# Optimization experiments

Hardware: AMD Instinct MI355X
Metric: run time of the kernel (lower is better)

Reference implementation:

```python
import jax, jax.numpy as jnp
import numpy as np

B, S, H, A = 32, 2048, 1024, 256
NEG = jnp.float32(-1e20)


def setup_inputs() -> dict:
    key = jax.random.key(0)
    k = jax.random.split(key, 6)
    h_i = jax.random.normal(k[0], (B, S, H), jnp.float32)
    h_t = jax.random.normal(k[1], (B, H), jnp.float32)
    mask = jax.random.randint(k[2], (B, S), 0, 2).astype(bool)
    W = jax.random.normal(k[3], (A, 2 * H), jnp.float32) * 0.02
    b = jax.random.normal(k[4], (A,), jnp.float32) * 0.02
    u = jax.random.normal(k[5], (A, 1), jnp.float32)
    return {"h_i": h_i, "h_t": h_t, "mask": mask, "W": W, "b": b, "u": u}


def reference(h_i, h_t, mask, W, b, u):
    Bn, Sn, Hn = h_i.shape
    # h_t expanded along seq and concatenated: [B,S,2H]
    h_t_e = jnp.broadcast_to(h_t[:, None, :], (Bn, Sn, Hn))
    comb = jnp.concatenate([h_i, h_t_e], axis=-1)
    m = jnp.tanh(jnp.einsum('bsk,ak->bsa', comb, W) + b)  # [B,S,A]
    y = jnp.einsum('bsa,a->bs', m, u[:, 0])                # raw scores [B,S]
    # Faithful replication of torch masked_scatter per time step over the batch
    # dim: at step s, the masked batch positions receive SUCCESSIVE elements of
    # the score column y[:, s] (not necessarily the positionally aligned ones).
    pos = jnp.clip(jnp.cumsum(mask.astype(jnp.int32), axis=0) - 1, 0)  # [B,S]
    y_scattered = jnp.take_along_axis(y, pos, axis=0)
    beta = jnp.where(mask, y_scattered, NEG)
    alpha = jax.nn.softmax(beta, axis=1)                   # softmax over seq
    s = jnp.einsum('bs,bsh->bh', alpha, h_i)               # weighted sum [B,H]
    return s
```

## Files before the change

### kernel.cpp

```cpp
#include <hip/hip_runtime.h>
#include <math.h>

#define BB 32
#define SS 2048
#define HH 1024
#define AA 256
#define NEGV (-1e20f)
#define BK 32
#define NT (HH / BK)
#define NG 16

typedef _Float16 half8 __attribute__((ext_vector_type(8)));
typedef float f32x4 __attribute__((ext_vector_type(4)));

__device__ inline void async_lds16(const void* g, void* l) {
    __builtin_amdgcn_global_load_lds(
        (const __attribute__((address_space(1))) unsigned int*)g,
        (__attribute__((address_space(3))) unsigned int*)l, 16, 0, 0);
}

__device__ inline f32x4 gload4(const float* p) {
    f32x4 r;
    asm volatile("global_load_dwordx4 %0, %1, off"
                 : "=&v"(r) : "v"(p) : "memory");
    return r;
}

__device__ inline half8 cvt8(f32x4 a, f32x4 b) {
    half8 h;
    h[0] = (_Float16)a[0]; h[1] = (_Float16)a[1];
    h[2] = (_Float16)a[2]; h[3] = (_Float16)a[3];
    h[4] = (_Float16)b[0]; h[5] = (_Float16)b[1];
    h[6] = (_Float16)b[2]; h[7] = (_Float16)b[3];
    return h;
}
__device__ inline half8 cvt8f(float4 a, float4 b) {
    half8 h;
    h[0] = (_Float16)a.x; h[1] = (_Float16)a.y;
    h[2] = (_Float16)a.z; h[3] = (_Float16)a.w;
    h[4] = (_Float16)b.x; h[5] = (_Float16)b.y;
    h[6] = (_Float16)b.z; h[7] = (_Float16)b.w;
    return h;
}

__global__ __launch_bounds__(256) void k_prep(const float* __restrict__ W,
                                              const float* __restrict__ h_t,
                                              const float* __restrict__ bias,
                                              const int* __restrict__ mask,
                                              _Float16* __restrict__ W16t,
                                              float* __restrict__ c,
                                              int* __restrict__ sList,
                                              int* __restrict__ cntb,
                                              int* __restrict__ pcnt,
                                              float* __restrict__ out) {
    const int blk = blockIdx.x;
    const int tid = threadIdx.x;
    __shared__ int lcnt;

    if (blk < 128) {
        int idx = blk * 256 + tid;
        int kt = idx >> 10;
        int u  = idx & 1023;
        int col = u >> 2, ks = u & 3;
        const float* src = W + (size_t)col * 2 * HH + kt * BK + ks * 8;
        float4 a0 = *(const float4*)src;
        float4 a1 = *(const float4*)(src + 4);
        *reinterpret_cast<half8*>(W16t + (size_t)idx * 8) = cvt8f(a0, a1);
        return;
    }
    if (blk < 2176) {
        int wave = tid >> 6;
        int lane = tid & 63;
        int pair = (blk - 128) * 4 + wave;
        int b = pair >> 8;
        int a = pair & (AA - 1);
        const float* ht = h_t + (size_t)b * HH;
        const float* w2 = W + (size_t)a * 2 * HH + HH;
        float acc = 0.f;
        for (int k = lane; k < HH; k += 64)
            acc += ht[k] * w2[k];
        for (int off = 32; off; off >>= 1)
            acc += __shfl_down(acc, off, 64);
        if (lane == 0) c[pair] = acc + bias[a];
        return;
    }
    if (blk >= 2208) {
        int i = (blk - 2208) * 256 + tid;
        *reinterpret_cast<f32x4*>(&out[(size_t)i * 4]) = (f32x4){0.f, 0.f, 0.f, 0.f};
        return;
    }
    const int b = blk - 2176;
    const int lane = tid & 63;
    if (tid == 0) lcnt = 0;
    __syncthreads();
    int* lst = sList + b * SS;
#pragma unroll
    for (int i = 0; i < 8; ++i) {
        int s = tid + i * 256;
        int pref = 0, tot = 0;
#pragma unroll
        for (int bb = 0; bb < BB; ++bb) {
            int mv = (mask[bb * SS + s] != 0);
            tot += mv;
            if (bb <= b) pref += mv;
        }
        pcnt[b * SS + s] = pref;
        bool need = (tot > b);
        unsigned long long mk = __ballot(need);
        int wbase = 0;
        if (lane == 0) wbase = atomicAdd(&lcnt, __popcll(mk));
        wbase = __shfl(wbase, 0, 64);
        if (need) lst[wbase + __popcll(mk & ((1ull << lane) - 1))] = s;
    }
    __syncthreads();
    const int m = lcnt;
    if (tid == 0) cntb[b] = m;
    if (m > 0) {
        int padded = (m + 63) & ~63;
        int first = lst[0];
        for (int j = m + tid; j < padded; j += 256) lst[j] = first;
    }
}

__global__ __launch_bounds__(256, 3) void k2_mfma(const float* __restrict__ h_i,
                                                  const _Float16* __restrict__ W16t,
                                                  const float* __restrict__ c,
                                                  const float* __restrict__ u,
                                                  const int* __restrict__ sList,
                                                  const int* __restrict__ cntb,
                                                  float* __restrict__ y) {
    __shared__ _Float16 Alds[3][4][64][8];
    __shared__ _Float16 Blds[2][1024][8];
    __shared__ float c_s[AA], u_s[AA];
    __shared__ float red[2][64];
    __shared__ int s_idx[64];

    const int t = blockIdx.x;
    int b = -1, ti = 0, base = 0;
    for (int bb = 0; bb < BB; ++bb) {
        int nt = (cntb[bb] + 63) >> 6;
        if (b < 0 && t < base + nt) { b = bb; ti = t - base; }
        base += nt;
    }
    if (b < 0) return;

    const int tid = threadIdx.x;
    const int lane = tid & 63;
    const int wave = tid >> 6;
    const int wr = wave >> 1;
    const int wc = wave & 1;

    if (tid < 64) s_idx[tid] = sList[b * SS + ti * 64 + tid];
    c_s[tid] = c[b * AA + tid];
    u_s[tid] = u[tid];
    __syncthreads();

    f32x4 acc[2][8];
#pragma unroll
    for (int rf = 0; rf < 2; ++rf)
#pragma unroll
        for (int cf = 0; cf < 8; ++cf) acc[rf][cf] = (f32x4){0.f, 0.f, 0.f, 0.f};

    const int arow = tid >> 2;
    const int aks = tid & 3;
    const float* Abase = h_i + ((size_t)b * SS + s_idx[arow]) * HH + aks * 8;

    const int sb0 = __builtin_amdgcn_readfirstlane(wave * 256);
    _Float16* Bflat = &Blds[0][0][0];

    const int kq = lane >> 4;
    const int lr = lane & 15;

    f32x4 r0a = gload4(Abase);
    f32x4 r0b = gload4(Abase + 4);
    f32x4 r1a = gload4(Abase + BK);
    f32x4 r1b = gload4(Abase + BK + 4);
#pragma unroll
    for (int i = 0; i < 4; ++i) {
        int sbase = sb0 + i * 64;
        async_lds16(W16t + (size_t)(sbase + lane) * 8, Bflat + (size_t)sbase * 8);
    }
    f32x4 rAa = gload4(Abase + 2 * BK);
    f32x4 rAb = gload4(Abase + 2 * BK + 4);

    asm volatile("s_waitcnt vmcnt(6)" ::: "memory");
    __builtin_amdgcn_sched_barrier(0);
    *reinterpret_cast<half8*>(&Alds[0][aks][arow][0]) = cvt8(r0a, r0b);
    *reinterpret_cast<half8*>(&Alds[1][aks][arow][0]) = cvt8(r1a, r1b);
    asm volatile("s_waitcnt vmcnt(2) lgkmcnt(0)" ::: "memory");
    __builtin_amdgcn_sched_barrier(0);
    __builtin_amdgcn_s_barrier();

    for (int t2 = 0; t2 < NT; ++t2) {
        const int cur3 = t2 % 3, curB = t2 & 1;
        if (t2 + 1 < NT) {
#pragma unroll
            for (int i = 0; i < 4; ++i) {
                int sbase = sb0 + i * 64;
                async_lds16(W16t + (size_t)(t2 + 1) * 8192 + (size_t)(sbase + lane) * 8,
                            Bflat + (size_t)((t2 + 1) & 1) * 8192 + (size_t)sbase * 8);
            }
        }
        if (t2 + 2 < NT) {
            asm volatile("s_waitcnt vmcnt(4)" ::: "memory");
            __builtin_amdgcn_sched_barrier(0);
            *reinterpret_cast<half8*>(&Alds[(t2 + 2) % 3][aks][arow][0]) = cvt8(rAa, rAb);
        }
        if (t2 + 3 < NT) {
            rAa = gload4(Abase + (t2 + 3) * BK);
            rAb = gload4(Abase + (t2 + 3) * BK + 4);
        }
        half8 af[2], bf[8];
#pragma unroll
        for (int rf = 0; rf < 2; ++rf)
            af[rf] = *reinterpret_cast<half8*>(&Alds[cur3][kq][wr * 32 + rf * 16 + lr][0]);
#pragma unroll
        for (int cf = 0; cf < 8; ++cf) {
            int col = wc * 128 + cf * 16 + lr;
            bf[cf] = *reinterpret_cast<half8*>(
                Bflat + (size_t)curB * 8192 + (size_t)(col * 4 + kq) * 8);
        }
        __builtin_amdgcn_s_setprio(1);
#pragma unroll
        for (int rf = 0; rf < 2; ++rf)
#pragma unroll
            for (int cf = 0; cf < 8; ++cf)
                acc[rf][cf] = __builtin_amdgcn_mfma_f32_16x16x32_f16(
                    af[rf], bf[cf], acc[rf][cf], 0, 0, 0);
        __builtin_amdgcn_s_setprio(0);
        if (t2 < NT - 1) {
            if (t2 + 3 < NT)
                asm volatile("s_waitcnt vmcnt(2) lgkmcnt(0)" ::: "memory");
            else
                asm volatile("s_waitcnt vmcnt(0) lgkmcnt(0)" ::: "memory");
            __builtin_amdgcn_sched_barrier(0);
            __builtin_amdgcn_s_barrier();
        }
    }

#pragma unroll
    for (int rf = 0; rf < 2; ++rf) {
#pragma unroll
        for (int j = 0; j < 4; ++j) {
            float v = 0.f;
#pragma unroll
            for (int cf = 0; cf < 8; ++cf) {
                int col = wc * 128 + cf * 16 + lr;
                float z = acc[rf][cf][j] + c_s[col];
                v += tanhf(z) * u_s[col];
            }
            v += __shfl_xor(v, 1, 64);
            v += __shfl_xor(v, 2, 64);
            v += __shfl_xor(v, 4, 64);
            v += __shfl_xor(v, 8, 64);
            if (lr == 0) red[wc][wr * 32 + rf * 16 + kq * 4 + j] = v;
        }
    }
    __syncthreads();
    if (tid < 64) y[(size_t)b * SS + s_idx[tid]] = red[0][tid] + red[1][tid];
}

__global__ __launch_bounds__(256) void k34(const float* __restrict__ h_i,
                                           const float* __restrict__ y,
                                           const int* __restrict__ mask,
                                           const int* __restrict__ pcnt,
                                           float* __restrict__ out) {
    const int blk = blockIdx.x;
    const int b = blk >> 4;
    const int grp = blk & (NG - 1);
    const int tid = threadIdx.x;
    const int lane = tid & 63;
    const int wave = tid >> 6;
    __shared__ float rmax[4], rsum[4];
    __shared__ float aval[128];
    __shared__ int slist[128];
    __shared__ int mtot;

    float beta[8];
    float mx = -INFINITY;
#pragma unroll
    for (int i = 0; i < 8; ++i) {
        int s = tid + i * 256;
        int p = pcnt[b * SS + s] - 1; if (p < 0) p = 0;
        float v = (mask[b * SS + s] != 0) ? y[(size_t)p * SS + s] : NEGV;
        beta[i] = v;
        mx = fmaxf(mx, v);
    }
    for (int off = 32; off; off >>= 1) mx = fmaxf(mx, __shfl_xor(mx, off, 64));
    if (lane == 0) rmax[wave] = mx;
    __syncthreads();
    mx = fmaxf(fmaxf(rmax[0], rmax[1]), fmaxf(rmax[2], rmax[3]));
    float sum = 0.f;
#pragma unroll
    for (int i = 0; i < 8; ++i) sum += expf(beta[i] - mx);
    for (int off = 32; off; off >>= 1) sum += __shfl_xor(sum, off, 64);
    if (lane == 0) rsum[wave] = sum;
    __syncthreads();
    sum = rsum[0] + rsum[1] + rsum[2] + rsum[3];
    const float inv = 1.f / sum;

    if (wave == 0) {
        int base = 0;
#pragma unroll
        for (int cc = 0; cc < 4; ++cc) {
            int s = grp * 128 + cc * 32 + lane;
            float a = 0.f;
            bool nz = false;
            if (lane < 32 && mask[b * SS + s] != 0) {
                int p = pcnt[b * SS + s] - 1; if (p < 0) p = 0;
                a = expf(y[(size_t)p * SS + s] - mx) * inv;
                nz = (a != 0.f);
            }
            unsigned long long mk = __ballot(nz);
            if (nz) {
                int off = base + __popcll(mk & ((1ull << lane) - 1));
                slist[off] = s;
                aval[off] = a;
            }
            base += __popcll(mk);
        }
        if (lane == 0) mtot = base;
    }
    __syncthreads();

    const int m = mtot;
    const float* basep = h_i + (size_t)b * SS * HH;
    f32x4 a0 = {0,0,0,0}, a1 = {0,0,0,0}, a2 = {0,0,0,0}, a3 = {0,0,0,0};
    int i2 = 0;
    for (; i2 + 4 <= m; i2 += 4) {
        float w0 = aval[i2],     w1 = aval[i2 + 1];
        float w2 = aval[i2 + 2], w3 = aval[i2 + 3];
        float4 v0 = *reinterpret_cast<const float4*>(&basep[(size_t)slist[i2]     * HH + tid * 4]);
        float4 v1 = *reinterpret_cast<const float4*>(&basep[(size_t)slist[i2 + 1] * HH + tid * 4]);
        float4 v2 = *reinterpret_cast<const float4*>(&basep[(size_t)slist[i2 + 2] * HH + tid * 4]);
        float4 v3 = *reinterpret_cast<const float4*>(&basep[(size_t)slist[i2 + 3] * HH + tid * 4]);
        a0[0] += w0 * v0.x; a0[1] += w0 * v0.y; a0[2] += w0 * v0.z; a0[3] += w0 * v0.w;
        a1[0] += w1 * v1.x; a1[1] += w1 * v1.y; a1[2] += w1 * v1.z; a1[3] += w1 * v1.w;
        a2[0] += w2 * v2.x; a2[1] += w2 * v2.y; a2[2] += w2 * v2.z; a2[3] += w2 * v2.w;
        a3[0] += w3 * v3.x; a3[1] += w3 * v3.y; a3[2] += w3 * v3.z; a3[3] += w3 * v3.w;
    }
    for (; i2 < m; ++i2) {
        float w0 = aval[i2];
        float4 v0 = *reinterpret_cast<const float4*>(&basep[(size_t)slist[i2] * HH + tid * 4]);
        a0[0] += w0 * v0.x; a0[1] += w0 * v0.y; a0[2] += w0 * v0.z; a0[3] += w0 * v0.w;
    }
    float r0 = (a0[0] + a1[0]) + (a2[0] + a3[0]);
    float r1 = (a0[1] + a1[1]) + (a2[1] + a3[1]);
    float r2 = (a0[2] + a1[2]) + (a2[2] + a3[2]);
    float r3 = (a0[3] + a1[3]) + (a2[3] + a3[3]);
    float* op = out + (size_t)b * HH + tid * 4;
    unsafeAtomicAdd(op + 0, r0);
    unsafeAtomicAdd(op + 1, r1);
    unsafeAtomicAdd(op + 2, r2);
    unsafeAtomicAdd(op + 3, r3);
}

extern "C" void kernel_launch(void* const* d_in, const int* in_sizes, int n_in,
                              void* d_out, int out_size, void* d_ws, size_t ws_size,
                              hipStream_t stream) {
    const float* h_i  = (const float*)d_in[0];
    const float* h_t  = (const float*)d_in[1];
    const int*   mask = (const int*)d_in[2];
    const float* W    = (const float*)d_in[3];
    const float* bias = (const float*)d_in[4];
    const float* u    = (const float*)d_in[5];
    float* out = (float*)d_out;

    float* c        = (float*)d_ws;
    float* y        = c + BB * AA;
    _Float16* W16t  = (_Float16*)(y + BB * SS);
    int* sList      = (int*)(W16t + AA * HH);
    int* cntb       = sList + BB * SS;
    int* pcnt       = cntb + BB;

    k_prep<<<2240, 256, 0, stream>>>(W, h_t, bias, mask, W16t, c, sList, cntb, pcnt, out);
    k2_mfma<<<1024, 256, 0, stream>>>(h_i, W16t, c, u, sList, cntb, y);
    k34<<<BB * NG, 256, 0, stream>>>(h_i, y, mask, pcnt, out);
}
```

Measured before the change: 97.91 us.

## Stage W slices in LDS for h_t projection and precompute masked score index

The bias-projection part of the prep kernel now uses 32 blocks. Each block loads 8 rows of the second half of W into shared memory once and loops over all batches, instead of 2048 blocks each reading a W row from global memory. The prep kernel also writes a combined index (mask folded into pcnt-1, or -1) so the softmax kernel reads one array instead of mask plus pcnt. The costs are a much smaller prep grid with a serial loop over batches, about 36KB of static LDS on every prep block, and extra __syncthreads per batch.

```diff
diff --git a/kernel.cpp b/kernel.cpp
--- a/kernel.cpp
+++ b/kernel.cpp
@@ -51,11 +51,15 @@
                                               float* __restrict__ c,
                                               int* __restrict__ sList,
                                               int* __restrict__ cntb,
-                                              int* __restrict__ pcnt,
+                                              int* __restrict__ yidx,
                                               float* __restrict__ out) {
     const int blk = blockIdx.x;
     const int tid = threadIdx.x;
+    const int lane = tid & 63;
+    const int wave = tid >> 6;
     __shared__ int lcnt;
+    __shared__ float w2s[8][HH];
+    __shared__ float hts[HH];
 
     if (blk < 128) {
         int idx = blk * 256 + tid;
@@ -68,29 +72,39 @@
         *reinterpret_cast<half8*>(W16t + (size_t)idx * 8) = cvt8f(a0, a1);
         return;
     }
-    if (blk < 2176) {
-        int wave = tid >> 6;
-        int lane = tid & 63;
-        int pair = (blk - 128) * 4 + wave;
-        int b = pair >> 8;
-        int a = pair & (AA - 1);
-        const float* ht = h_t + (size_t)b * HH;
-        const float* w2 = W + (size_t)a * 2 * HH + HH;
-        float acc = 0.f;
-        for (int k = lane; k < HH; k += 64)
-            acc += ht[k] * w2[k];
-        for (int off = 32; off; off >>= 1)
-            acc += __shfl_down(acc, off, 64);
-        if (lane == 0) c[pair] = acc + bias[a];
+    if (blk < 160) {
+        const int a0 = (blk - 128) * 8;
+        for (int i = tid; i < 8 * (HH / 4); i += 256) {
+            int a_l = i >> 8;
+            int kc = (i & 255) * 4;
+            *reinterpret_cast<float4*>(&w2s[a_l][kc]) =
+                *reinterpret_cast<const float4*>(&W[(size_t)(a0 + a_l) * 2 * HH + HH + kc]);
+        }
+        for (int b = 0; b < BB; ++b) {
+            __syncthreads();
+            for (int i = tid; i < HH / 4; i += 256)
+                *reinterpret_cast<float4*>(&hts[i * 4]) =
+                    *reinterpret_cast<const float4*>(&h_t[(size_t)b * HH + i * 4]);
+            __syncthreads();
+#pragma unroll
+            for (int aw = 0; aw < 2; ++aw) {
+                int a_l = wave * 2 + aw;
+                float acc = 0.f;
+                for (int k = lane; k < HH; k += 64)
+                    acc += w2s[a_l][k] * hts[k];
+                for (int off = 32; off; off >>= 1)
+                    acc += __shfl_down(acc, off, 64);
+                if (lane == 0) c[b * AA + a0 + a_l] = acc + bias[a0 + a_l];
+            }
+        }
         return;
     }
-    if (blk >= 2208) {
-        int i = (blk - 2208) * 256 + tid;
+    if (blk >= 192) {
+        int i = (blk - 192) * 256 + tid;
         *reinterpret_cast<f32x4*>(&out[(size_t)i * 4]) = (f32x4){0.f, 0.f, 0.f, 0.f};
         return;
     }
-    const int b = blk - 2176;
-    const int lane = tid & 63;
+    const int b = blk - 160;
     if (tid == 0) lcnt = 0;
     __syncthreads();
     int* lst = sList + b * SS;
@@ -104,7 +118,7 @@
             tot += mv;
             if (bb <= b) pref += mv;
         }
-        pcnt[b * SS + s] = pref;
+        yidx[b * SS + s] = (mask[b * SS + s] != 0) ? (pref - 1) : -1;
         bool need = (tot > b);
         unsigned long long mk = __ballot(need);
         int wbase = 0;
@@ -262,8 +276,7 @@
 
 __global__ __launch_bounds__(256) void k34(const float* __restrict__ h_i,
                                            const float* __restrict__ y,
-                                           const int* __restrict__ mask,
-                                           const int* __restrict__ pcnt,
+                                           const int* __restrict__ yidx,
                                            float* __restrict__ out) {
     const int blk = blockIdx.x;
     const int b = blk >> 4;
@@ -281,8 +294,9 @@
 #pragma unroll
     for (int i = 0; i < 8; ++i) {
         int s = tid + i * 256;
-        int p = pcnt[b * SS + s] - 1; if (p < 0) p = 0;
-        float v = (mask[b * SS + s] != 0) ? y[(size_t)p * SS + s] : NEGV;
+        int p = yidx[b * SS + s];
+        int pc = p < 0 ? 0 : p;
+        float v = (p >= 0) ? y[(size_t)pc * SS + s] : NEGV;
         beta[i] = v;
         mx = fmaxf(mx, v);
     }
@@ -306,10 +320,12 @@
             int s = grp * 128 + cc * 32 + lane;
             float a = 0.f;
             bool nz = false;
-            if (lane < 32 && mask[b * SS + s] != 0) {
-                int p = pcnt[b * SS + s] - 1; if (p < 0) p = 0;
-                a = expf(y[(size_t)p * SS + s] - mx) * inv;
-                nz = (a != 0.f);
+            if (lane < 32) {
+                int p = yidx[b * SS + s];
+                if (p >= 0) {
+                    a = expf(y[(size_t)p * SS + s] - mx) * inv;
+                    nz = (a != 0.f);
+                }
             }
             unsigned long long mk = __ballot(nz);
             if (nz) {
@@ -371,9 +387,9 @@
     _Float16* W16t  = (_Float16*)(y + BB * SS);
     int* sList      = (int*)(W16t + AA * HH);
     int* cntb       = sList + BB * SS;
-    int* pcnt       = cntb + BB;
-
-    k_prep<<<2240, 256, 0, stream>>>(W, h_t, bias, mask, W16t, c, sList, cntb, pcnt, out);
+    int* yidx       = cntb + BB;
+
+    k_prep<<<224, 256, 0, stream>>>(W, h_t, bias, mask, W16t, c, sList, cntb, yidx, out);
     k2_mfma<<<1024, 256, 0, stream>>>(h_i, W16t, c, u, sList, cntb, y);
-    k34<<<BB * NG, 256, 0, stream>>>(h_i, y, mask, pcnt, out);
-}
+    k34<<<BB * NG, 256, 0, stream>>>(h_i, y, yidx, out);
+}
```

New measurement: 151.0 us. 1.54x slower.
